# Optimization experiments

Measured on AMD Instinct MI355X. Metric: run time of the kernel, lower is better.

The kernel has to match this reference:

```python
import jax, jax.numpy as jnp
import numpy as np

N = 20000      # nodes
E = 160000     # edges (avg degree 16)
IN_DIM = 256
HID = 128      # hidden_dim == per-head out_channels in PyG TransformerConv
HEADS = 4
EPS = 1e-5


def setup_inputs() -> dict:
    key = jax.random.key(0)
    ks = jax.random.split(key, 24)

    def w(k, shape, scale=0.05):
        return jax.random.normal(k, shape, dtype=jnp.float32) * scale

    inp = {
        "x": jax.random.normal(ks[0], (N, IN_DIM), dtype=jnp.float32),
        "edge_index": jax.random.randint(ks[1], (2, E), 0, N, dtype=jnp.int32),
        # input projection
        "lin_w": w(ks[2], (IN_DIM, HID)), "lin_b": jnp.zeros((HID,), jnp.float32),
    }
    i = 3
    for l in (1, 2):
        inp[f"q_w{l}"] = w(ks[i], (HID, HEADS * HID)); i += 1
        inp[f"q_b{l}"] = jnp.zeros((HEADS * HID,), jnp.float32)
        inp[f"k_w{l}"] = w(ks[i], (HID, HEADS * HID)); i += 1
        inp[f"k_b{l}"] = jnp.zeros((HEADS * HID,), jnp.float32)
        inp[f"v_w{l}"] = w(ks[i], (HID, HEADS * HID)); i += 1
        inp[f"v_b{l}"] = jnp.zeros((HEADS * HID,), jnp.float32)
        inp[f"s_w{l}"] = w(ks[i], (HID, HID)); i += 1
        inp[f"s_b{l}"] = jnp.zeros((HID,), jnp.float32)
        inp[f"ln_g{l}"] = jnp.ones((HID,), jnp.float32)
        inp[f"ln_b{l}"] = jnp.zeros((HID,), jnp.float32)
    return inp


def _segment_softmax(scores, seg, num):
    # scores: [E, HEADS], seg: [E] destination indices
    m = jax.ops.segment_max(scores, seg, num_segments=num)
    m = jnp.where(jnp.isfinite(m), m, 0.0)  # guard empty segments
    e = jnp.exp(scores - m[seg])
    d = jax.ops.segment_sum(e, seg, num_segments=num)
    return e / (d[seg] + 1e-16)


def _transformer_conv(x, src, dst, qw, qb, kw, kb, vw, vb, sw, sb):
    # PyG TransformerConv(HID, HID, heads=HEADS, concat=False)
    n = x.shape[0]
    q = (x @ qw + qb).reshape(n, HEADS, HID)
    k = (x @ kw + kb).reshape(n, HEADS, HID)
    v = (x @ vw + vb).reshape(n, HEADS, HID)
    # per-edge attention: query at dst (i), key/value at src (j)
    alpha = jnp.einsum("ehd,ehd->eh", q[dst], k[src]) / jnp.sqrt(jnp.float32(HID))
    alpha = _segment_softmax(alpha, dst, n)                 # [E, HEADS]
    msg = v[src] * alpha[..., None]                          # [E, HEADS, HID]
    out = jax.ops.segment_sum(msg, dst, num_segments=n)      # [N, HEADS, HID]
    out = out.mean(axis=1)                                   # concat=False -> head mean
    return out + x @ sw + sb                                 # root skip connection


def _layer_norm(x, g, b):
    mu = x.mean(-1, keepdims=True)
    var = ((x - mu) ** 2).mean(-1, keepdims=True)
    return (x - mu) * jax.lax.rsqrt(var + EPS) * g + b


def reference(x, edge_index, lin_w, lin_b,
              q_w1, q_b1, k_w1, k_b1, v_w1, v_b1, s_w1, s_b1, ln_g1, ln_b1,
              q_w2, q_b2, k_w2, k_b2, v_w2, v_b2, s_w2, s_b2, ln_g2, ln_b2):
    src, dst = edge_index[0], edge_index[1]
    h = jax.nn.relu(x @ lin_w + lin_b)
    h1 = _transformer_conv(h, src, dst, q_w1, q_b1, k_w1, k_b1, v_w1, v_b1, s_w1, s_b1)
    h = _layer_norm(h1 + h, ln_g1, ln_b1)
    h2 = _transformer_conv(h, src, dst, q_w2, q_b2, k_w2, k_b2, v_w2, v_b2, s_w2, s_b2)
    h = _layer_norm(h2 + h, ln_g2, ln_b2)
    return h
```

## Files before the change

### kernel.cpp

```cpp
#include <hip/hip_runtime.h>
#include <math.h>

#define NNODE 20000
#define NEDGE 160000
#define IN_DIMV 256
#define HIDV 128
#define DEGCAP 64
#define BAT 4

typedef __attribute__((ext_vector_type(8))) short bf16x8;
typedef __attribute__((ext_vector_type(4))) float f32x4;
typedef __attribute__((ext_vector_type(2))) float f32x2;

__device__ __forceinline__ float bf2f(unsigned short u) {
    union { unsigned int i; float f; } x; x.i = ((unsigned int)u) << 16; return x.f;
}
__device__ __forceinline__ unsigned short f2bf(float f) {
    union { float f; unsigned int i; } x; x.f = f;
    unsigned int r = x.i + 0x7fffu + ((x.i >> 16) & 1u);
    return (unsigned short)(r >> 16);
}
__device__ __forceinline__ void unpack8(uint4 p, float* f) {
    f[0] = bf2f((unsigned short)(p.x & 0xffff)); f[1] = bf2f((unsigned short)(p.x >> 16));
    f[2] = bf2f((unsigned short)(p.y & 0xffff)); f[3] = bf2f((unsigned short)(p.y >> 16));
    f[4] = bf2f((unsigned short)(p.z & 0xffff)); f[5] = bf2f((unsigned short)(p.z >> 16));
    f[6] = bf2f((unsigned short)(p.w & 0xffff)); f[7] = bf2f((unsigned short)(p.w >> 16));
}
__device__ __forceinline__ void unpack8f8_w(unsigned int a, unsigned int b, float* f) {
    f32x2 t;
    t = __builtin_amdgcn_cvt_pk_f32_fp8((int)a, false); f[0] = t.x; f[1] = t.y;
    t = __builtin_amdgcn_cvt_pk_f32_fp8((int)a, true);  f[2] = t.x; f[3] = t.y;
    t = __builtin_amdgcn_cvt_pk_f32_fp8((int)b, false); f[4] = t.x; f[5] = t.y;
    t = __builtin_amdgcn_cvt_pk_f32_fp8((int)b, true);  f[6] = t.x; f[7] = t.y;
}
__device__ __forceinline__ unsigned char f2fp8(float v) {
    int pk = __builtin_amdgcn_cvt_pk_fp8_f32(v, v, 0, false);
    return (unsigned char)(pk & 0xff);
}
__device__ __forceinline__ void gld_lds16(const unsigned short* g, unsigned short* l) {
    __builtin_amdgcn_global_load_lds((const __attribute__((address_space(1))) void*)g,
                                     (__attribute__((address_space(3))) void*)l, 16, 0, 0);
}

__global__ void convert_kernel(
    const float* __restrict__ lin_w,
    const float* __restrict__ qw0, const float* __restrict__ kw0,
    const float* __restrict__ vw0, const float* __restrict__ sw0,
    const float* __restrict__ qw1, const float* __restrict__ kw1,
    const float* __restrict__ vw1, const float* __restrict__ sw1,
    unsigned short* __restrict__ arena, int* __restrict__ cursor)
{
    int idx = blockIdx.x * 256 + threadIdx.x;
    if (idx < NNODE) cursor[idx] = 0;
    int id2 = idx - NNODE;
    if (id2 < 0 || id2 >= 458752) return;
    float v;
    if (id2 < 32768) {
        int n = id2 >> 8, k = id2 & 255;
        v = lin_w[k * 128 + n];
    } else {
        int t = id2 - 32768;
        int l = t / 212992, r = t % 212992;
        int n = r >> 7, k = r & 127;
        const float* qw = l ? qw1 : qw0;
        const float* kw = l ? kw1 : kw0;
        const float* vw = l ? vw1 : vw0;
        const float* sw = l ? sw1 : sw0;
        if (n < 1536) {
            const float* w = (n < 512) ? qw : (n < 1024) ? kw : vw;
            v = w[k * 512 + (n & 511)];
        } else {
            v = sw[k * 128 + (n - 1536)];
        }
    }
    arena[id2] = f2bf(v);
}

__global__ __launch_bounds__(256) void mfma_gemm0(
    const float* __restrict__ A, const unsigned short* __restrict__ WT,
    const float* __restrict__ b0, unsigned short* __restrict__ hbf_out)
{
    __shared__ unsigned short smem[8192];
    unsigned short* As = smem;
    unsigned short* Bs = smem + 4096;
    unsigned short* ot = smem;
    const int K = 256;

    int tid = threadIdx.x;
    int lane = tid & 63;
    int w = tid >> 6;
    int wm = w & 1, wn = w >> 1;
    int bm = blockIdx.x * 128;

    int r0 = tid >> 2;
    int c0 = (tid & 3) * 8;
    int g0 = bm + r0;      if (g0 > NNODE - 1) g0 = NNODE - 1;
    int g1 = bm + r0 + 64; if (g1 > NNODE - 1) g1 = NNODE - 1;
    int srow = lane >> 2;
    int scol = (lane & 3) * 8;
    int br0 = w * 32 + srow;
    int br1 = w * 32 + 16 + srow;

    f32x4 acc[4][4] = {};
    int arow = wm * 64 + (lane & 15);
    int brow = wn * 64 + (lane & 15);
    int koff = (lane >> 4) * 8;

    for (int k0 = 0; k0 < K; k0 += 32) {
        {
            const float4* p0 = (const float4*)(A + (size_t)g0 * K + k0 + c0);
            float4 u = p0[0], v = p0[1];
            unsigned short t0[8] = {f2bf(u.x), f2bf(u.y), f2bf(u.z), f2bf(u.w),
                                    f2bf(v.x), f2bf(v.y), f2bf(v.z), f2bf(v.w)};
            *(uint4*)&As[r0 * 32 + c0] = *(uint4*)t0;
            const float4* p1 = (const float4*)(A + (size_t)g1 * K + k0 + c0);
            u = p1[0]; v = p1[1];
            unsigned short t1[8] = {f2bf(u.x), f2bf(u.y), f2bf(u.z), f2bf(u.w),
                                    f2bf(v.x), f2bf(v.y), f2bf(v.z), f2bf(v.w)};
            *(uint4*)&As[(r0 + 64) * 32 + c0] = *(uint4*)t1;
        }
        gld_lds16(WT + (size_t)br0 * K + k0 + scol, Bs + (w * 32) * 32);
        gld_lds16(WT + (size_t)br1 * K + k0 + scol, Bs + (w * 32 + 16) * 32);
        __syncthreads();
        bf16x8 fa[4], fb[4];
#pragma unroll
        for (int i = 0; i < 4; i++) fa[i] = *(const bf16x8*)&As[(arow + i * 16) * 32 + koff];
#pragma unroll
        for (int i = 0; i < 4; i++) fb[i] = *(const bf16x8*)&Bs[(brow + i * 16) * 32 + koff];
#pragma unroll
        for (int mi = 0; mi < 4; mi++)
#pragma unroll
            for (int ni = 0; ni < 4; ni++)
                acc[mi][ni] = __builtin_amdgcn_mfma_f32_16x16x32_bf16(fa[mi], fb[ni], acc[mi][ni], 0, 0, 0);
        __syncthreads();
    }

    int quad = lane >> 4, lcol = lane & 15;
#pragma unroll
    for (int hh = 0; hh < 2; hh++) {
        __syncthreads();
        if (wm == hh) {
#pragma unroll
            for (int mi = 0; mi < 4; mi++) {
#pragma unroll
                for (int ni = 0; ni < 4; ni++) {
                    int lc = wn * 64 + ni * 16 + lcol;
                    float bias = b0[lc];
#pragma unroll
                    for (int reg = 0; reg < 4; reg++) {
                        float v = fmaxf(acc[mi][ni][reg] + bias, 0.f);
                        ot[(mi * 16 + quad * 4 + reg) * 128 + lc] = f2bf(v);
                    }
                }
            }
        }
        __syncthreads();
        int r = tid >> 2, ch = tid & 3;
        int row = bm + hh * 64 + r;
        if (row < NNODE) {
            uint4* dp = (uint4*)(hbf_out + (size_t)row * HIDV + ch * 32);
            const uint4* sp = (const uint4*)(ot + r * 128 + ch * 32);
#pragma unroll
            for (int q = 0; q < 4; q++) dp[q] = sp[q];
        }
    }
}

__global__ __launch_bounds__(256) void mfma_gemm1(
    const unsigned short* __restrict__ A, const unsigned short* __restrict__ WT,
    const float* __restrict__ b0, const float* __restrict__ b1,
    const float* __restrict__ b2, const float* __restrict__ b3,
    unsigned short* __restrict__ qb_out, unsigned char* __restrict__ kv8_out,
    unsigned short* __restrict__ pre16_out)
{
    __shared__ unsigned short As[16384];
    __shared__ unsigned short Ws[16384];
    unsigned short* ot = Ws;
    unsigned char* ot8 = (unsigned char*)Ws;
    const int K = 128;

    int tid = threadIdx.x;
    int lane = tid & 63;
    int w = tid >> 6;
    int wm = w & 1, wn = w >> 1;
    int bm = blockIdx.x * 128;
    int p0 = (blockIdx.y == 0) ? 0 : 7;
    int p1 = (blockIdx.y == 0) ? 7 : 13;

    int srow = lane >> 2;
    int scol = (lane & 3) * 8;
    int sr0 = w * 32 + srow;
    int sr1 = w * 32 + 16 + srow;
    int ar0 = bm + sr0; if (ar0 > NNODE - 1) ar0 = NNODE - 1;
    int ar1 = bm + sr1; if (ar1 > NNODE - 1) ar1 = NNODE - 1;

#pragma unroll
    for (int c = 0; c < 4; c++) {
        int k0 = c * 32;
        gld_lds16(A + (size_t)ar0 * K + k0 + scol, As + c * 4096 + sr0 * 32);
        gld_lds16(A + (size_t)ar1 * K + k0 + scol, As + c * 4096 + sr1 * 32);
    }

    int arow = wm * 64 + (lane & 15);
    int brow = wn * 64 + (lane & 15);
    int koff = (lane >> 4) * 8;
    int quad = lane >> 4, lcol = lane & 15;

    for (int p = p0; p < p1; p++) {
        int bn = p * 128;
#pragma unroll
        for (int c = 0; c < 4; c++) {
            int k0 = c * 32;
            gld_lds16(WT + (size_t)(bn + sr0) * K + k0 + scol, Ws + c * 4096 + sr0 * 32);
            gld_lds16(WT + (size_t)(bn + sr1) * K + k0 + scol, Ws + c * 4096 + sr1 * 32);
        }
        __syncthreads();

        f32x4 acc[4][4] = {};
#pragma unroll
        for (int c = 0; c < 4; c++) {
            bf16x8 fa[4], fb[4];
#pragma unroll
            for (int i = 0; i < 4; i++) fa[i] = *(const bf16x8*)&As[c * 4096 + (arow + i * 16) * 32 + koff];
#pragma unroll
            for (int i = 0; i < 4; i++) fb[i] = *(const bf16x8*)&Ws[c * 4096 + (brow + i * 16) * 32 + koff];
#pragma unroll
            for (int mi = 0; mi < 4; mi++)
#pragma unroll
                for (int ni = 0; ni < 4; ni++)
                    acc[mi][ni] = __builtin_amdgcn_mfma_f32_16x16x32_bf16(fa[mi], fb[ni], acc[mi][ni], 0, 0, 0);
        }
        __syncthreads();

        if (p < 4 || p == 12) {
            const float* bb = (p < 4) ? (b0 + bn) : b3;
#pragma unroll
            for (int mi = 0; mi < 4; mi++) {
#pragma unroll
                for (int ni = 0; ni < 4; ni++) {
                    int lc = wn * 64 + ni * 16 + lcol;
                    float bias = bb[lc];
#pragma unroll
                    for (int reg = 0; reg < 4; reg++)
                        ot[(wm * 64 + mi * 16 + quad * 4 + reg) * 128 + lc] = f2bf(acc[mi][ni][reg] + bias);
                }
            }
            __syncthreads();
            int r = tid >> 1, hf = tid & 1;
            int row = bm + r;
            if (row < NNODE) {
                unsigned short* dst = (p < 4) ? (qb_out + (size_t)row * 512 + bn + hf * 64)
                                              : (pre16_out + (size_t)row * HIDV + hf * 64);
                const uint4* sp = (const uint4*)(ot + r * 128 + hf * 64);
                uint4* dp = (uint4*)dst;
#pragma unroll
                for (int q = 0; q < 8; q++) dp[q] = sp[q];
            }
            __syncthreads();
        } else {
            const float* bb = (bn < 1024) ? (b1 + bn - 512) : (b2 + bn - 1024);
            int coff = bn - 512;
#pragma unroll
            for (int mi = 0; mi < 4; mi++) {
#pragma unroll
                for (int ni = 0; ni < 4; ni++) {
                    int lc = wn * 64 + ni * 16 + lcol;
                    float bias = bb[lc];
#pragma unroll
                    for (int reg = 0; reg < 4; reg++)
                        ot8[(wm * 64 + mi * 16 + quad * 4 + reg) * 128 + lc] = f2fp8(acc[mi][ni][reg] + bias);
                }
            }
            __syncthreads();
            int r = tid >> 1, hf = tid & 1;
            int row = bm + r;
            if (row < NNODE) {
                uint4* dp = (uint4*)(kv8_out + (size_t)row * 1024 + coff + hf * 64);
                const uint4* sp = (const uint4*)(ot8 + r * 128 + hf * 64);
#pragma unroll
                for (int q = 0; q < 4; q++) dp[q] = sp[q];
            }
            __syncthreads();
        }
    }
}

__global__ void scatter_kernel(const int* __restrict__ ei, int* __restrict__ cursor,
                               int* __restrict__ bucket) {
    int e = blockIdx.x * blockDim.x + threadIdx.x;
    if (e < NEDGE) {
        int d = ei[NEDGE + e];
        int slot = atomicAdd(&cursor[d], 1);
        if (slot < DEGCAP) bucket[d * DEGCAP + slot] = ei[e];
    }
}

__global__ __launch_bounds__(256) void attn_ln_kernel(
    const unsigned short* __restrict__ qb, const unsigned char* __restrict__ kv8,
    const int* __restrict__ cursor, const int* __restrict__ bucket,
    const unsigned short* __restrict__ pre16, const float* __restrict__ g,
    const float* __restrict__ b,
    unsigned short* __restrict__ hbf ,
    float* __restrict__ extout)
{
    int lane = threadIdx.x & 63;
    int wid = threadIdx.x >> 6;
    int i = blockIdx.x * 4 + wid;
    int cnt = cursor[i]; if (cnt > DEGCAP) cnt = DEGCAP;
    const int* bk = bucket + i * DEGCAP;

    int hg = lane >> 4;
    int sl = lane & 15;
    int off = hg * 128 + sl * 8;

    size_t base = (size_t)i * HIDV + sl * 8;
    uint4 pv_raw = *(const uint4*)(pre16 + base);
    uint4 hv_raw = *(const uint4*)(hbf + base);

    float qr[8];
    {
        uint4 p = *(const uint4*)(qb + (size_t)i * 512 + lane * 8);
        unpack8(p, qr);
#pragma unroll
        for (int j = 0; j < 8; j++) qr[j] *= 0.0883883476483184f;
    }

    float m = -INFINITY, l = 0.f;
    float acc[8] = {0.f, 0.f, 0.f, 0.f, 0.f, 0.f, 0.f, 0.f};

    if (cnt > 0) {
        int myidx = bk[(lane < cnt) ? lane : 0];

        uint2 kA[BAT], vA[BAT], kB[BAT], vB[BAT];

        auto issue = [&](uint2 (&KB)[BAT], uint2 (&VB)[BAT], int bb) {
#pragma unroll
            for (int t = 0; t < BAT; t++) {
                int j = bb * BAT + t; if (j >= cnt) j = cnt - 1;
                int src = __shfl(myidx, j);
                const unsigned char* bp = kv8 + (size_t)src * 1024 + off;
                KB[t] = *(const uint2*)bp;
                VB[t] = *(const uint2*)(bp + 512);
            }
        };

        auto consume = [&](const uint2 (&KB)[BAT], const uint2 (&VB)[BAT], int bb) {
            int rem = cnt - bb * BAT;
            float d[BAT];
#pragma unroll
            for (int t = 0; t < BAT; t++) d[t] = -3.0e38f;
#pragma unroll
            for (int t = 0; t < BAT; t++) {
                if (t >= rem) break;
                float kf[8];
                unpack8f8_w(KB[t].x, KB[t].y, kf);
                d[t] = qr[0] * kf[0] + qr[1] * kf[1] + qr[2] * kf[2] + qr[3] * kf[3] +
                       qr[4] * kf[4] + qr[5] * kf[5] + qr[6] * kf[6] + qr[7] * kf[7];
            }
#pragma unroll
            for (int t = 0; t < BAT; t++) { if (t >= rem) break; d[t] += __shfl_xor(d[t], 8); }
#pragma unroll
            for (int t = 0; t < BAT; t++) { if (t >= rem) break; d[t] += __shfl_xor(d[t], 4); }
#pragma unroll
            for (int t = 0; t < BAT; t++) { if (t >= rem) break; d[t] += __shfl_xor(d[t], 2); }
#pragma unroll
            for (int t = 0; t < BAT; t++) { if (t >= rem) break; d[t] += __shfl_xor(d[t], 1); }

            float mq = d[0];
#pragma unroll
            for (int t = 1; t < BAT; t++) mq = fmaxf(mq, d[t]);
            float mn = fmaxf(m, mq);
            float scale = __expf(m - mn);
            float p[BAT];
            float psum = 0.f;
#pragma unroll
            for (int t = 0; t < BAT; t++) { p[t] = __expf(d[t] - mn); psum += p[t]; }
            l = l * scale + psum;
            m = mn;
#pragma unroll
            for (int c = 0; c < 8; c++) acc[c] *= scale;
#pragma unroll
            for (int t = 0; t < BAT; t++) {
                if (t >= rem) break;
                float vf[8];
                unpack8f8_w(VB[t].x, VB[t].y, vf);
                float pt = p[t];
#pragma unroll
                for (int c = 0; c < 8; c++) acc[c] += pt * vf[c];
            }
        };

        int nb = (cnt + BAT - 1) >> 2;
        issue(kA, vA, 0);
        for (int bb = 0; bb < nb; bb += 2) {
            if (bb + 1 < nb) issue(kB, vB, bb + 1);
            consume(kA, vA, bb);
            if (bb + 1 < nb) {
                if (bb + 2 < nb) issue(kA, vA, bb + 2);
                consume(kB, vB, bb + 1);
            }
        }
    }

    float linv = 0.25f / (l + 1e-16f);
#pragma unroll
    for (int c = 0; c < 8; c++) acc[c] *= linv;
#pragma unroll
    for (int c = 0; c < 8; c++) {
        acc[c] += __shfl_xor(acc[c], 16);
        acc[c] += __shfl_xor(acc[c], 32);
    }

    float pv[8], hv[8];
    unpack8(pv_raw, pv);
    unpack8(hv_raw, hv);
    float vals[8];
#pragma unroll
    for (int c = 0; c < 8; c++) vals[c] = acc[c] + pv[c] + hv[c];

    float s = 0.f;
#pragma unroll
    for (int c = 0; c < 8; c++) s += vals[c];
    s += __shfl_xor(s, 1); s += __shfl_xor(s, 2);
    s += __shfl_xor(s, 4); s += __shfl_xor(s, 8);
    float mu = s * (1.f / 128.f);
    float vs = 0.f;
#pragma unroll
    for (int c = 0; c < 8; c++) { float dx = vals[c] - mu; vs += dx * dx; }
    vs += __shfl_xor(vs, 1); vs += __shfl_xor(vs, 2);
    vs += __shfl_xor(vs, 4); vs += __shfl_xor(vs, 8);
    float rstd = rsqrtf(vs * (1.f / 128.f) + 1e-5f);

    float4 g0 = ((const float4*)(g + sl * 8))[0];
    float4 g1 = ((const float4*)(g + sl * 8))[1];
    float4 bb0 = ((const float4*)(b + sl * 8))[0];
    float4 bb1 = ((const float4*)(b + sl * 8))[1];
    float y[8];
    y[0] = (vals[0] - mu) * rstd * g0.x + bb0.x; y[1] = (vals[1] - mu) * rstd * g0.y + bb0.y;
    y[2] = (vals[2] - mu) * rstd * g0.z + bb0.z; y[3] = (vals[3] - mu) * rstd * g0.w + bb0.w;
    y[4] = (vals[4] - mu) * rstd * g1.x + bb1.x; y[5] = (vals[5] - mu) * rstd * g1.y + bb1.y;
    y[6] = (vals[6] - mu) * rstd * g1.z + bb1.z; y[7] = (vals[7] - mu) * rstd * g1.w + bb1.w;

    if (lane < 16) {
        unsigned short tmp[8] = {f2bf(y[0]), f2bf(y[1]), f2bf(y[2]), f2bf(y[3]),
                                 f2bf(y[4]), f2bf(y[5]), f2bf(y[6]), f2bf(y[7])};
        *(uint4*)(hbf + base) = *(uint4*)tmp;
        if (extout) {
            ((float4*)(extout + base))[0] = make_float4(y[0], y[1], y[2], y[3]);
            ((float4*)(extout + base))[1] = make_float4(y[4], y[5], y[6], y[7]);
        }
    }
}

extern "C" void kernel_launch(void* const* d_in, const int* in_sizes, int n_in,
                              void* d_out, int out_size, void* d_ws, size_t ws_size,
                              hipStream_t stream) {
    const float* x = (const float*)d_in[0];
    const int* ei = (const int*)d_in[1];

    char* ws = (char*)d_ws;
    unsigned short* hbf = (unsigned short*)(ws + 0);
    unsigned short* pre16 = (unsigned short*)(ws + 5120000);
    unsigned short* qb = (unsigned short*)(ws + 10240000);
    unsigned char* kv8 = (unsigned char*)(ws + 30720000);
    int* cursor = (int*)(ws + 51200000);
    int* bucket = (int*)(ws + 51280000);
    unsigned short* arena = (unsigned short*)(ws + 56400000);

    convert_kernel<<<(NNODE + 458752 + 255) / 256, 256, 0, stream>>>(
        (const float*)d_in[2],
        (const float*)d_in[4], (const float*)d_in[6], (const float*)d_in[8], (const float*)d_in[10],
        (const float*)d_in[14], (const float*)d_in[16], (const float*)d_in[18], (const float*)d_in[20],
        arena, cursor);

    scatter_kernel<<<(NEDGE + 255) / 256, 256, 0, stream>>>(ei, cursor, bucket);

    const int GM = (NNODE + 127) / 128;

    mfma_gemm0<<<GM, 256, 0, stream>>>(x, arena, (const float*)d_in[3], hbf);

    for (int l = 0; l < 2; l++) {
        int o = 4 + l * 10;
        const unsigned short* WT = arena + 32768 + l * 212992;
        mfma_gemm1<<<dim3(GM, 2), 256, 0, stream>>>(
            hbf, WT,
            (const float*)d_in[o + 1], (const float*)d_in[o + 3],
            (const float*)d_in[o + 5], (const float*)d_in[o + 7],
            qb, kv8, pre16);

        attn_ln_kernel<<<NNODE / 4, 256, 0, stream>>>(
            qb, kv8, cursor, bucket, pre16,
            (const float*)d_in[o + 8], (const float*)d_in[o + 9],
            hbf, (l == 1) ? (float*)d_out : nullptr);
    }
}
```

Baseline: 279.5 us.

## Shrink fused QKV GEMM row tile to 64 and hoist bucket index load

The QKV/skip projection GEMM now uses 64-row M tiles instead of 128, and each of the four waves computes a 64x32 slice of the 128-wide output tile. This doubles the grid so the 20000-node problem fills more CUs, cuts LDS and accumulator registers per block, and shrinks the epilogue. The cost is reloading the weight tiles twice as often across blocks. Separately, the attention kernel now loads each lane's neighbor index unconditionally before the count check, so that load overlaps with the other prologue loads. This reads bucket slots beyond the count, which may hold uninitialised values that are never used.

```diff
diff --git a/kernel.cpp b/kernel.cpp
--- a/kernel.cpp
+++ b/kernel.cpp
@@ -173,7 +173,7 @@
     unsigned short* __restrict__ qb_out, unsigned char* __restrict__ kv8_out,
     unsigned short* __restrict__ pre16_out)
 {
-    __shared__ unsigned short As[16384];
+    __shared__ unsigned short As[8192];
     __shared__ unsigned short Ws[16384];
     unsigned short* ot = Ws;
     unsigned char* ot8 = (unsigned char*)Ws;
@@ -182,27 +182,23 @@
     int tid = threadIdx.x;
     int lane = tid & 63;
     int w = tid >> 6;
-    int wm = w & 1, wn = w >> 1;
-    int bm = blockIdx.x * 128;
+    int bm = blockIdx.x * 64;
     int p0 = (blockIdx.y == 0) ? 0 : 7;
     int p1 = (blockIdx.y == 0) ? 7 : 13;
 
     int srow = lane >> 2;
     int scol = (lane & 3) * 8;
+    int asr = w * 16 + srow;
+    int aar = bm + asr; if (aar > NNODE - 1) aar = NNODE - 1;
     int sr0 = w * 32 + srow;
     int sr1 = w * 32 + 16 + srow;
-    int ar0 = bm + sr0; if (ar0 > NNODE - 1) ar0 = NNODE - 1;
-    int ar1 = bm + sr1; if (ar1 > NNODE - 1) ar1 = NNODE - 1;
 
 #pragma unroll
     for (int c = 0; c < 4; c++) {
-        int k0 = c * 32;
-        gld_lds16(A + (size_t)ar0 * K + k0 + scol, As + c * 4096 + sr0 * 32);
-        gld_lds16(A + (size_t)ar1 * K + k0 + scol, As + c * 4096 + sr1 * 32);
-    }
-
-    int arow = wm * 64 + (lane & 15);
-    int brow = wn * 64 + (lane & 15);
+        gld_lds16(A + (size_t)aar * K + c * 32 + scol, As + c * 2048 + asr * 32);
+    }
+
+    int arow = lane & 15;
     int koff = (lane >> 4) * 8;
     int quad = lane >> 4, lcol = lane & 15;
 
@@ -210,24 +206,23 @@
         int bn = p * 128;
 #pragma unroll
         for (int c = 0; c < 4; c++) {
-            int k0 = c * 32;
-            gld_lds16(WT + (size_t)(bn + sr0) * K + k0 + scol, Ws + c * 4096 + sr0 * 32);
-            gld_lds16(WT + (size_t)(bn + sr1) * K + k0 + scol, Ws + c * 4096 + sr1 * 32);
-        }
-        __syncthreads();
-
-        f32x4 acc[4][4] = {};
+            gld_lds16(WT + (size_t)(bn + sr0) * K + c * 32 + scol, Ws + c * 4096 + sr0 * 32);
+            gld_lds16(WT + (size_t)(bn + sr1) * K + c * 32 + scol, Ws + c * 4096 + sr1 * 32);
+        }
+        __syncthreads();
+
+        f32x4 acc[4][2] = {};
 #pragma unroll
         for (int c = 0; c < 4; c++) {
-            bf16x8 fa[4], fb[4];
-#pragma unroll
-            for (int i = 0; i < 4; i++) fa[i] = *(const bf16x8*)&As[c * 4096 + (arow + i * 16) * 32 + koff];
-#pragma unroll
-            for (int i = 0; i < 4; i++) fb[i] = *(const bf16x8*)&Ws[c * 4096 + (brow + i * 16) * 32 + koff];
+            bf16x8 fa[4], fb[2];
+#pragma unroll
+            for (int i = 0; i < 4; i++) fa[i] = *(const bf16x8*)&As[c * 2048 + (arow + i * 16) * 32 + koff];
+#pragma unroll
+            for (int i = 0; i < 2; i++) fb[i] = *(const bf16x8*)&Ws[c * 4096 + (w * 32 + i * 16 + arow) * 32 + koff];
 #pragma unroll
             for (int mi = 0; mi < 4; mi++)
 #pragma unroll
-                for (int ni = 0; ni < 4; ni++)
+                for (int ni = 0; ni < 2; ni++)
                     acc[mi][ni] = __builtin_amdgcn_mfma_f32_16x16x32_bf16(fa[mi], fb[ni], acc[mi][ni], 0, 0, 0);
         }
         __syncthreads();
@@ -237,24 +232,24 @@
 #pragma unroll
             for (int mi = 0; mi < 4; mi++) {
 #pragma unroll
-                for (int ni = 0; ni < 4; ni++) {
-                    int lc = wn * 64 + ni * 16 + lcol;
+                for (int ni = 0; ni < 2; ni++) {
+                    int lc = w * 32 + ni * 16 + lcol;
                     float bias = bb[lc];
 #pragma unroll
                     for (int reg = 0; reg < 4; reg++)
-                        ot[(wm * 64 + mi * 16 + quad * 4 + reg) * 128 + lc] = f2bf(acc[mi][ni][reg] + bias);
+                        ot[(mi * 16 + quad * 4 + reg) * 128 + lc] = f2bf(acc[mi][ni][reg] + bias);
                 }
             }
             __syncthreads();
-            int r = tid >> 1, hf = tid & 1;
+            int r = tid >> 2, q = tid & 3;
             int row = bm + r;
             if (row < NNODE) {
-                unsigned short* dst = (p < 4) ? (qb_out + (size_t)row * 512 + bn + hf * 64)
-                                              : (pre16_out + (size_t)row * HIDV + hf * 64);
-                const uint4* sp = (const uint4*)(ot + r * 128 + hf * 64);
+                unsigned short* dst = (p < 4) ? (qb_out + (size_t)row * 512 + bn + q * 32)
+                                              : (pre16_out + (size_t)row * HIDV + q * 32);
+                const uint4* sp = (const uint4*)(ot + r * 128 + q * 32);
                 uint4* dp = (uint4*)dst;
 #pragma unroll
-                for (int q = 0; q < 8; q++) dp[q] = sp[q];
+                for (int qq = 0; qq < 4; qq++) dp[qq] = sp[qq];
             }
             __syncthreads();
         } else {
@@ -263,22 +258,21 @@
 #pragma unroll
             for (int mi = 0; mi < 4; mi++) {
 #pragma unroll
-                for (int ni = 0; ni < 4; ni++) {
-                    int lc = wn * 64 + ni * 16 + lcol;
+                for (int ni = 0; ni < 2; ni++) {
+                    int lc = w * 32 + ni * 16 + lcol;
                     float bias = bb[lc];
 #pragma unroll
                     for (int reg = 0; reg < 4; reg++)
-                        ot8[(wm * 64 + mi * 16 + quad * 4 + reg) * 128 + lc] = f2fp8(acc[mi][ni][reg] + bias);
+                        ot8[(mi * 16 + quad * 4 + reg) * 128 + lc] = f2fp8(acc[mi][ni][reg] + bias);
                 }
             }
             __syncthreads();
-            int r = tid >> 1, hf = tid & 1;
+            int r = tid >> 2, q = tid & 3;
             int row = bm + r;
             if (row < NNODE) {
-                uint4* dp = (uint4*)(kv8_out + (size_t)row * 1024 + coff + hf * 64);
-                const uint4* sp = (const uint4*)(ot8 + r * 128 + hf * 64);
-#pragma unroll
-                for (int q = 0; q < 4; q++) dp[q] = sp[q];
+                uint4* dp = (uint4*)(kv8_out + (size_t)row * 1024 + coff + q * 32);
+                const uint4* sp = (const uint4*)(ot8 + r * 128 + q * 32);
+                dp[0] = sp[0]; dp[1] = sp[1];
             }
             __syncthreads();
         }
@@ -306,8 +300,8 @@
     int lane = threadIdx.x & 63;
     int wid = threadIdx.x >> 6;
     int i = blockIdx.x * 4 + wid;
+    int myidx = bucket[i * DEGCAP + lane];
     int cnt = cursor[i]; if (cnt > DEGCAP) cnt = DEGCAP;
-    const int* bk = bucket + i * DEGCAP;
 
     int hg = lane >> 4;
     int sl = lane & 15;
@@ -329,8 +323,6 @@
     float acc[8] = {0.f, 0.f, 0.f, 0.f, 0.f, 0.f, 0.f, 0.f};
 
     if (cnt > 0) {
-        int myidx = bk[(lane < cnt) ? lane : 0];
-
         uint2 kA[BAT], vA[BAT], kB[BAT], vB[BAT];
 
         auto issue = [&](uint2 (&KB)[BAT], uint2 (&VB)[BAT], int bb) {
@@ -476,13 +468,14 @@
     scatter_kernel<<<(NEDGE + 255) / 256, 256, 0, stream>>>(ei, cursor, bucket);
 
     const int GM = (NNODE + 127) / 128;
+    const int GM64 = (NNODE + 63) / 64;
 
     mfma_gemm0<<<GM, 256, 0, stream>>>(x, arena, (const float*)d_in[3], hbf);
 
     for (int l = 0; l < 2; l++) {
         int o = 4 + l * 10;
         const unsigned short* WT = arena + 32768 + l * 212992;
-        mfma_gemm1<<<dim3(GM, 2), 256, 0, stream>>>(
+        mfma_gemm1<<<dim3(GM64, 2), 256, 0, stream>>>(
             hbf, WT,
             (const float*)d_in[o + 1], (const float*)d_in[o + 3],
             (const float*)d_in[o + 5], (const float*)d_in[o + 7],
```

Result: faster. 271.9 us (-2.7%).
